# Performance work log

Measured on AMD Instinct MI355X. Metric: run time of the kernel, lower is better.

Reference implementation:

```python
import jax, jax.numpy as jnp
import numpy as np

MARGIN_POS = 0.1
MARGIN_NEG = 0.8
HARD_RATIO = 0.3


def setup_inputs() -> dict:
    key = jax.random.key(0)
    k1, k2, k3 = jax.random.split(key, 3)
    B, D = 16384, 1024
    return {
        "q_neg_proj": jax.random.normal(k1, (B, D), dtype=jnp.float32),
        "d_pos": jax.random.normal(k2, (B, D), dtype=jnp.float32),
        "d_neg": jax.random.normal(k3, (B, D), dtype=jnp.float32),
    }


def reference(q_neg_proj, d_pos, d_neg):
    B = q_neg_proj.shape[0]
    num_hard = max(1, int(B * HARD_RATIO))

    # diag(q @ d.T) == rowwise dot product; avoid the BxB matmul
    diag_sim_pos = jnp.einsum("bd,bd->b", q_neg_proj, d_pos)
    diag_sim_neg = jnp.einsum("bd,bd->b", q_neg_proj, d_neg)

    # hardest positives: largest similarities
    hard_sim_pos, _ = jax.lax.top_k(diag_sim_pos, num_hard)
    loss_pos = jnp.mean(jax.nn.relu(hard_sim_pos - MARGIN_POS))

    # hardest negatives: smallest similarities (topk largest=False)
    neg_smallest, _ = jax.lax.top_k(-diag_sim_neg, num_hard)
    hard_sim_neg = -neg_smallest
    loss_neg = jnp.mean(jax.nn.relu(MARGIN_NEG - hard_sim_neg))

    total_loss = loss_pos + loss_neg
    return (total_loss, loss_pos, loss_neg)
```

## Files before the change

kernel.cpp:

```cpp
#include <hip/hip_runtime.h>

constexpr int B_ROWS = 16384;
constexpr int K_HARD = 4915;
constexpr float MARGIN_POS = 0.1f;
constexpr float MARGIN_NEG = 0.8f;

typedef float f32x4 __attribute__((ext_vector_type(4)));

__global__ __launch_bounds__(256, 8) void dot_kernel(
    const float* __restrict__ q,
    const float* __restrict__ dp,
    const float* __restrict__ dn,
    float* __restrict__ out_pos,
    float* __restrict__ out_neg)
{
    const int wave = (blockIdx.x * blockDim.x + threadIdx.x) >> 6;
    const int lane = threadIdx.x & 63;
    const unsigned voff = (unsigned)wave * 4096u + (unsigned)lane * 16u;

    f32x4 q0, q1, q2, q3, p0, p1, p2, p3, n0, n1, n2, n3;
    asm volatile(
        "global_load_dwordx4 %[Q0], %[VO], %[QB] offset:0\n\t"
        "global_load_dwordx4 %[Q1], %[VO], %[QB] offset:1024\n\t"
        "global_load_dwordx4 %[Q2], %[VO], %[QB] offset:2048\n\t"
        "global_load_dwordx4 %[Q3], %[VO], %[QB] offset:3072\n\t"
        "global_load_dwordx4 %[P0], %[VO], %[PB] offset:0\n\t"
        "global_load_dwordx4 %[P1], %[VO], %[PB] offset:1024\n\t"
        "global_load_dwordx4 %[P2], %[VO], %[PB] offset:2048\n\t"
        "global_load_dwordx4 %[P3], %[VO], %[PB] offset:3072\n\t"
        "global_load_dwordx4 %[N0], %[VO], %[NB] offset:0\n\t"
        "global_load_dwordx4 %[N1], %[VO], %[NB] offset:1024\n\t"
        "global_load_dwordx4 %[N2], %[VO], %[NB] offset:2048\n\t"
        "global_load_dwordx4 %[N3], %[VO], %[NB] offset:3072\n\t"
        "s_waitcnt vmcnt(0)"
        : [Q0]"=&v"(q0), [Q1]"=&v"(q1), [Q2]"=&v"(q2), [Q3]"=&v"(q3),
          [P0]"=&v"(p0), [P1]"=&v"(p1), [P2]"=&v"(p2), [P3]"=&v"(p3),
          [N0]"=&v"(n0), [N1]"=&v"(n1), [N2]"=&v"(n2), [N3]"=&v"(n3)
        : [VO]"v"(voff), [QB]"s"(q), [PB]"s"(dp), [NB]"s"(dn)
    );

    f32x4 qa[4] = {q0, q1, q2, q3};
    f32x4 pa[4] = {p0, p1, p2, p3};
    f32x4 na[4] = {n0, n1, n2, n3};

    float sp = 0.f, sn = 0.f;
#pragma unroll
    for (int it = 0; it < 4; ++it) {
#pragma unroll
        for (int c = 0; c < 4; ++c) {
            sp += qa[it][c] * pa[it][c];
            sn += qa[it][c] * na[it][c];
        }
    }
#pragma unroll
    for (int off = 32; off; off >>= 1) {
        sp += __shfl_xor(sp, off);
        sn += __shfl_xor(sn, off);
    }
    if (lane == 0) {
        out_pos[wave] = sp;
        out_neg[wave] = sn;
    }
}

__device__ __forceinline__ unsigned f2key(float f) {
    unsigned u = __float_as_uint(f);
    return (u & 0x80000000u) ? ~u : (u | 0x80000000u);
}
__device__ __forceinline__ float key2f(unsigned k) {
    return __uint_as_float((k & 0x80000000u) ? (k & 0x7FFFFFFFu) : ~k);
}

__global__ __launch_bounds__(1024) void select_finalize_kernel(
    const float* __restrict__ ws_vals,
    float* __restrict__ out)
{
    __shared__ unsigned hist[2][256];
    __shared__ unsigned ebase[2][256];
    __shared__ unsigned s_prefix[2], s_m[2];
    __shared__ float    s_rf[2][16];
    __shared__ unsigned s_rc[2][16];

    const int tid  = threadIdx.x;
    const int lane = tid & 63;
    const int wid  = tid >> 6;

    const float4* vp = (const float4*)ws_vals;
    const float4* vn = (const float4*)(ws_vals + B_ROWS);

    unsigned kp[16], kn[16];
#pragma unroll
    for (int j = 0; j < 4; ++j) {
        const float4 a = vp[tid + j * 1024];
        const float4 b = vn[tid + j * 1024];
        kp[4*j+0] = f2key(a.x); kp[4*j+1] = f2key(a.y);
        kp[4*j+2] = f2key(a.z); kp[4*j+3] = f2key(a.w);
        kn[4*j+0] = f2key(b.x); kn[4*j+1] = f2key(b.y);
        kn[4*j+2] = f2key(b.z); kn[4*j+3] = f2key(b.w);
    }

    unsigned m0 = (unsigned)(B_ROWS - K_HARD), pre0 = 0;
    unsigned m1 = (unsigned)(K_HARD - 1),      pre1 = 0;

    for (int r = 0; r < 4; ++r) {
        const unsigned shift = 24 - 8 * r;
        const unsigned pmask = (r == 0) ? 0u : (0xFFFFFFFFu << (32 - 8 * r));
        if (tid < 256) { hist[0][tid] = 0; hist[1][tid] = 0; }
        __syncthreads();
#pragma unroll
        for (int j = 0; j < 16; ++j) {
            if ((kp[j] & pmask) == pre0) atomicAdd(&hist[0][(kp[j] >> shift) & 255u], 1u);
            if ((kn[j] & pmask) == pre1) atomicAdd(&hist[1][(kn[j] >> shift) & 255u], 1u);
        }
        __syncthreads();

        if (wid < 2) {
            const int s = wid;
            const unsigned h0 = hist[s][4*lane+0], h1 = hist[s][4*lane+1];
            const unsigned h2 = hist[s][4*lane+2], h3 = hist[s][4*lane+3];
            const unsigned g = h0 + h1 + h2 + h3;
            unsigned inc = g;
#pragma unroll
            for (int off = 1; off < 64; off <<= 1) {
                const unsigned t = __shfl_up(inc, off);
                if (lane >= off) inc += t;
            }
            const unsigned ex = inc - g;
            ebase[s][4*lane+0] = ex;
            ebase[s][4*lane+1] = ex + h0;
            ebase[s][4*lane+2] = ex + h0 + h1;
            ebase[s][4*lane+3] = ex + h0 + h1 + h2;
        }
        __syncthreads();

        if (tid < 512) {
            const int s = tid >> 8;
            const int b = tid & 255;
            const unsigned mm = s ? m1 : m0;
            const unsigned lo = ebase[s][b];
            const unsigned hi = lo + hist[s][b];
            if (lo <= mm && mm < hi) {
                s_prefix[s] = (s ? pre1 : pre0) | ((unsigned)b << shift);
                s_m[s] = mm - lo;
            }
        }
        __syncthreads();
        pre0 = s_prefix[0]; m0 = s_m[0];
        pre1 = s_prefix[1]; m1 = s_m[1];
    }

    const unsigned tk0 = pre0, tk1 = pre1;
    const float    tv0 = key2f(tk0), tv1 = key2f(tk1);

    float lp = 0.f, ln = 0.f;
    unsigned cp = 0, cn = 0;
#pragma unroll
    for (int j = 0; j < 16; ++j) {
        if (kp[j] > tk0) { lp += fmaxf(key2f(kp[j]) - MARGIN_POS, 0.f); cp++; }
        if (kn[j] < tk1) { ln += fmaxf(MARGIN_NEG - key2f(kn[j]), 0.f); cn++; }
    }
#pragma unroll
    for (int off = 32; off; off >>= 1) {
        lp += __shfl_xor(lp, off);  ln += __shfl_xor(ln, off);
        cp += __shfl_xor(cp, off);  cn += __shfl_xor(cn, off);
    }
    if (lane == 0) {
        s_rf[0][wid] = lp; s_rf[1][wid] = ln;
        s_rc[0][wid] = cp; s_rc[1][wid] = cn;
    }
    __syncthreads();
    if (tid == 0) {
        float tp = 0.f, tn = 0.f;
        unsigned ccp = 0, ccn = 0;
        for (int w = 0; w < 16; ++w) {
            tp += s_rf[0][w]; tn += s_rf[1][w];
            ccp += s_rc[0][w]; ccn += s_rc[1][w];
        }
        const float fp = fmaxf(tv0 - MARGIN_POS, 0.f);
        const float fn = fmaxf(MARGIN_NEG - tv1, 0.f);
        const float LP = (tp + (float)(K_HARD - (int)ccp) * fp) / (float)K_HARD;
        const float LN = (tn + (float)(K_HARD - (int)ccn) * fn) / (float)K_HARD;
        out[0] = LP + LN;
        out[1] = LP;
        out[2] = LN;
    }
}

extern "C" void kernel_launch(void* const* d_in, const int* in_sizes, int n_in,
                              void* d_out, int out_size, void* d_ws, size_t ws_size,
                              hipStream_t stream) {
    const float* q  = (const float*)d_in[0];
    const float* dp = (const float*)d_in[1];
    const float* dn = (const float*)d_in[2];
    float* out = (float*)d_out;

    float* ws     = (float*)d_ws;
    float* ws_pos = ws;
    float* ws_neg = ws + B_ROWS;

    dot_kernel<<<(B_ROWS * 64) / 256, 256, 0, stream>>>(q, dp, dn, ws_pos, ws_neg);
    select_finalize_kernel<<<1, 1024, 0, stream>>>(ws_pos, out);
}
```

Measured before the change: 52.79 us.

## Process four rows per wave with double-buffered register prefetch

Each wave now processes four rows strided by 4096, keeping two row-sets of loads in flight and waiting only on the older batch before computing its dot products. The grid shrinks fourfold and launch bounds are relaxed to allow more registers per thread. This aims to keep more memory requests outstanding per wave and reduce per-block overhead. The cost is fewer resident waves and higher register pressure.

```diff
diff --git a/kernel.cpp b/kernel.cpp
--- a/kernel.cpp
+++ b/kernel.cpp
@@ -7,18 +7,15 @@
 
 typedef float f32x4 __attribute__((ext_vector_type(4)));
 
-__global__ __launch_bounds__(256, 8) void dot_kernel(
-    const float* __restrict__ q,
-    const float* __restrict__ dp,
-    const float* __restrict__ dn,
-    float* __restrict__ out_pos,
-    float* __restrict__ out_neg)
-{
-    const int wave = (blockIdx.x * blockDim.x + threadIdx.x) >> 6;
-    const int lane = threadIdx.x & 63;
-    const unsigned voff = (unsigned)wave * 4096u + (unsigned)lane * 16u;
-
+struct RowRegs {
     f32x4 q0, q1, q2, q3, p0, p1, p2, p3, n0, n1, n2, n3;
+};
+
+__device__ __forceinline__ void issue12(RowRegs& r, unsigned vo,
+                                        const float* __restrict__ q,
+                                        const float* __restrict__ dp,
+                                        const float* __restrict__ dn)
+{
     asm volatile(
         "global_load_dwordx4 %[Q0], %[VO], %[QB] offset:0\n\t"
         "global_load_dwordx4 %[Q1], %[VO], %[QB] offset:1024\n\t"
@@ -31,35 +28,74 @@
         "global_load_dwordx4 %[N0], %[VO], %[NB] offset:0\n\t"
         "global_load_dwordx4 %[N1], %[VO], %[NB] offset:1024\n\t"
         "global_load_dwordx4 %[N2], %[VO], %[NB] offset:2048\n\t"
-        "global_load_dwordx4 %[N3], %[VO], %[NB] offset:3072\n\t"
-        "s_waitcnt vmcnt(0)"
-        : [Q0]"=&v"(q0), [Q1]"=&v"(q1), [Q2]"=&v"(q2), [Q3]"=&v"(q3),
-          [P0]"=&v"(p0), [P1]"=&v"(p1), [P2]"=&v"(p2), [P3]"=&v"(p3),
-          [N0]"=&v"(n0), [N1]"=&v"(n1), [N2]"=&v"(n2), [N3]"=&v"(n3)
-        : [VO]"v"(voff), [QB]"s"(q), [PB]"s"(dp), [NB]"s"(dn)
+        "global_load_dwordx4 %[N3], %[VO], %[NB] offset:3072"
+        : [Q0]"=&v"(r.q0), [Q1]"=&v"(r.q1), [Q2]"=&v"(r.q2), [Q3]"=&v"(r.q3),
+          [P0]"=&v"(r.p0), [P1]"=&v"(r.p1), [P2]"=&v"(r.p2), [P3]"=&v"(r.p3),
+          [N0]"=&v"(r.n0), [N1]"=&v"(r.n1), [N2]"=&v"(r.n2), [N3]"=&v"(r.n3)
+        : [VO]"v"(vo), [QB]"s"(q), [PB]"s"(dp), [NB]"s"(dn)
     );
-
-    f32x4 qa[4] = {q0, q1, q2, q3};
-    f32x4 pa[4] = {p0, p1, p2, p3};
-    f32x4 na[4] = {n0, n1, n2, n3};
-
-    float sp = 0.f, sn = 0.f;
-#pragma unroll
-    for (int it = 0; it < 4; ++it) {
-#pragma unroll
-        for (int c = 0; c < 4; ++c) {
-            sp += qa[it][c] * pa[it][c];
-            sn += qa[it][c] * na[it][c];
-        }
-    }
+}
+
+#define WAITV12 do { asm volatile("s_waitcnt vmcnt(12)" ::: "memory"); \
+                     __builtin_amdgcn_sched_barrier(0); } while (0)
+#define WAITV0  do { asm volatile("s_waitcnt vmcnt(0)"  ::: "memory"); \
+                     __builtin_amdgcn_sched_barrier(0); } while (0)
+
+__device__ __forceinline__ void dot2(const RowRegs& r, float& sp, float& sn)
+{
+    float a = 0.f, b = 0.f;
+#pragma unroll
+    for (int c = 0; c < 4; ++c) {
+        a += r.q0[c] * r.p0[c]; b += r.q0[c] * r.n0[c];
+        a += r.q1[c] * r.p1[c]; b += r.q1[c] * r.n1[c];
+        a += r.q2[c] * r.p2[c]; b += r.q2[c] * r.n2[c];
+        a += r.q3[c] * r.p3[c]; b += r.q3[c] * r.n3[c];
+    }
+    sp = a; sn = b;
+}
+
+__global__ __launch_bounds__(256, 4) void dot_kernel(
+    const float* __restrict__ q,
+    const float* __restrict__ dp,
+    const float* __restrict__ dn,
+    float* __restrict__ out_pos,
+    float* __restrict__ out_neg)
+{
+    const int NW   = 4096;
+    const int wave = (blockIdx.x * blockDim.x + threadIdx.x) >> 6;
+    const int lane = threadIdx.x & 63;
+
+    const unsigned vo0  = (unsigned)wave * 4096u + (unsigned)lane * 16u;
+    const unsigned step = (unsigned)NW * 4096u;
+
+    RowRegs A, B;
+    float sp0, sn0, sp1, sn1, sp2, sn2, sp3, sn3;
+
+    issue12(A, vo0,            q, dp, dn);
+    issue12(B, vo0 + step,     q, dp, dn);
+    WAITV12;
+    dot2(A, sp0, sn0);
+    issue12(A, vo0 + 2 * step, q, dp, dn);
+    WAITV12;
+    dot2(B, sp1, sn1);
+    issue12(B, vo0 + 3 * step, q, dp, dn);
+    WAITV12;
+    dot2(A, sp2, sn2);
+    WAITV0;
+    dot2(B, sp3, sn3);
+
 #pragma unroll
     for (int off = 32; off; off >>= 1) {
-        sp += __shfl_xor(sp, off);
-        sn += __shfl_xor(sn, off);
+        sp0 += __shfl_xor(sp0, off); sn0 += __shfl_xor(sn0, off);
+        sp1 += __shfl_xor(sp1, off); sn1 += __shfl_xor(sn1, off);
+        sp2 += __shfl_xor(sp2, off); sn2 += __shfl_xor(sn2, off);
+        sp3 += __shfl_xor(sp3, off); sn3 += __shfl_xor(sn3, off);
     }
     if (lane == 0) {
-        out_pos[wave] = sp;
-        out_neg[wave] = sn;
+        out_pos[wave]          = sp0;  out_neg[wave]          = sn0;
+        out_pos[wave + NW]     = sp1;  out_neg[wave + NW]     = sn1;
+        out_pos[wave + 2*NW]   = sp2;  out_neg[wave + 2*NW]   = sn2;
+        out_pos[wave + 3*NW]   = sp3;  out_neg[wave + 3*NW]   = sn3;
     }
 }
 
@@ -198,6 +234,6 @@
     float* ws_pos = ws;
     float* ws_neg = ws + B_ROWS;
 
-    dot_kernel<<<(B_ROWS * 64) / 256, 256, 0, stream>>>(q, dp, dn, ws_pos, ws_neg);
+    dot_kernel<<<1024, 256, 0, stream>>>(q, dp, dn, ws_pos, ws_neg);
     select_finalize_kernel<<<1, 1024, 0, stream>>>(ws_pos, out);
 }
```

New measurement: 52.94 us. Within noise of the previous version (+0.3%).
